# Performance work log

Measured on AMD Instinct MI355X. Metric: run time of the kernel, lower is better.

## Reference

```python
import jax, jax.numpy as jnp
import numpy as np

B = 8192
IN = 2048
H = 2048


def setup_inputs() -> dict:
    key = jax.random.key(0)
    ks = jax.random.split(key, 16)
    s_in = 1.0 / np.sqrt(IN)
    s_h = 1.0 / np.sqrt(H)
    inp = {
        "x": jax.random.normal(ks[0], (B, IN), jnp.float32),
        "h": jax.random.normal(ks[1], (B, H), jnp.float32),
        "c": jax.random.normal(ks[2], (B, H), jnp.float32),
        # Linear weights stored torch-style as [out, in]
        "w_xf": jax.random.uniform(ks[3], (H, IN), jnp.float32, -s_in, s_in),
        "w_hf": jax.random.uniform(ks[4], (H, H), jnp.float32, -s_h, s_h),
        "b_f": jax.random.normal(ks[5], (H,), jnp.float32),
        "w_xi": jax.random.uniform(ks[6], (H, IN), jnp.float32, -s_in, s_in),
        "w_hi": jax.random.uniform(ks[7], (H, H), jnp.float32, -s_h, s_h),
        "b_i": jax.random.normal(ks[8], (H,), jnp.float32),
        "w_xo": jax.random.uniform(ks[9], (H, IN), jnp.float32, -s_in, s_in),
        "w_ho": jax.random.uniform(ks[10], (H, H), jnp.float32, -s_h, s_h),
        "b_o": jax.random.normal(ks[11], (H,), jnp.float32),
        "w_xc": jax.random.uniform(ks[12], (H, IN), jnp.float32, -s_in, s_in),
        "w_hc": jax.random.uniform(ks[13], (H, H), jnp.float32, -s_h, s_h),
        "b_c": jax.random.normal(ks[14], (H,), jnp.float32),
    }
    return inp


def reference(x, h, c, w_xf, w_hf, b_f, w_xi, w_hi, b_i,
              w_xo, w_ho, b_o, w_xc, w_hc, b_c):
    # Fuse the 8 small GEMMs into 2 batched GEMMs (x-side, h-side).
    Wx = jnp.concatenate([w_xf, w_xi, w_xo, w_xc], axis=0)  # [4H, IN]
    Wh = jnp.concatenate([w_hf, w_hi, w_ho, w_hc], axis=0)  # [4H, H]
    b = jnp.concatenate([b_f, b_i, b_o, b_c], axis=0)       # [4H]
    gates = x @ Wx.T + h @ Wh.T + b                          # [B, 4H]
    hd = h.shape[-1]
    f = jax.nn.sigmoid(gates[:, 0 * hd:1 * hd])
    i = jax.nn.sigmoid(gates[:, 1 * hd:2 * hd])
    o = jax.nn.sigmoid(gates[:, 2 * hd:3 * hd])
    c_tilde = jnp.tanh(gates[:, 3 * hd:4 * hd])
    c_new = f * c + i * c_tilde
    h_new = o * jnp.tanh(c_new)
    return (h_new, c_new)
```

## Files before the change

kernel.cpp:

```cpp
#include <hip/hip_runtime.h>


typedef __attribute__((ext_vector_type(8))) short short8;
typedef __attribute__((ext_vector_type(8))) __bf16 bf16x8;
typedef __attribute__((ext_vector_type(4))) float f32x4;

#define GLDS(gp, lp)                                                        \
  __builtin_amdgcn_global_load_lds(                                         \
      (const __attribute__((address_space(1))) void*)(gp),                  \
      (__attribute__((address_space(3))) void*)(lp), 16, 0, 0)

__device__ __forceinline__ unsigned short f2bf(float f) {
  unsigned u = __builtin_bit_cast(unsigned, f);
  u = (u + 0x7FFFu + ((u >> 16) & 1u)) >> 16;
  return (unsigned short)u;
}

__global__ void pack_x_kernel(const float* __restrict__ x,
                              const float* __restrict__ h,
                              short* __restrict__ X2) {
  long tid = (long)blockIdx.x * blockDim.x + threadIdx.x;
  long flat = tid * 8;
  int row = (int)(flat >> 12);
  int k = (int)(flat & 4095);
  const float* src = (k < 2048) ? (x + (long)row * 2048 + k)
                                : (h + (long)row * 2048 + (k - 2048));
  float4 a = *(const float4*)src;
  float4 b = *(const float4*)(src + 4);
  short8 o;
  o[0] = (short)f2bf(a.x); o[1] = (short)f2bf(a.y);
  o[2] = (short)f2bf(a.z); o[3] = (short)f2bf(a.w);
  o[4] = (short)f2bf(b.x); o[5] = (short)f2bf(b.y);
  o[6] = (short)f2bf(b.z); o[7] = (short)f2bf(b.w);
  *(short8*)(X2 + flat) = o;
}

__global__ void pack_w_kernel(const float* __restrict__ wxf, const float* __restrict__ wxi,
                              const float* __restrict__ wxo, const float* __restrict__ wxc,
                              const float* __restrict__ whf, const float* __restrict__ whi,
                              const float* __restrict__ who, const float* __restrict__ whc,
                              short* __restrict__ W3) {
  long tid = (long)blockIdx.x * blockDim.x + threadIdx.x;
  long flat = tid * 8;
  int j = (int)(flat >> 12);
  int k = (int)(flat & 4095);
  int hc = ((j >> 6) << 4) | (j & 15);
  int g = (j >> 4) & 3;
  const float* base;
  if (k < 2048) {
    const float* wx = (g == 0) ? wxf : (g == 1) ? wxi : (g == 2) ? wxo : wxc;
    base = wx + (long)hc * 2048 + k;
  } else {
    const float* wh = (g == 0) ? whf : (g == 1) ? whi : (g == 2) ? who : whc;
    base = wh + (long)hc * 2048 + (k - 2048);
  }
  float4 a = *(const float4*)base;
  float4 b = *(const float4*)(base + 4);
  short8 o;
  o[0] = (short)f2bf(a.x); o[1] = (short)f2bf(a.y);
  o[2] = (short)f2bf(a.z); o[3] = (short)f2bf(a.w);
  o[4] = (short)f2bf(b.x); o[5] = (short)f2bf(b.y);
  o[6] = (short)f2bf(b.z); o[7] = (short)f2bf(b.w);
  *(short8*)(W3 + flat) = o;
}

__global__ __launch_bounds__(512, 2) void lstm_fused_gemm(
    const short* __restrict__ X2, const short* __restrict__ W3,
    const float* __restrict__ cin,
    const float* __restrict__ bF, const float* __restrict__ bI,
    const float* __restrict__ bO, const float* __restrict__ bC,
    float* __restrict__ hout, float* __restrict__ cout_) {
  __shared__ __align__(16) short lds[65536];

  const int tid = threadIdx.x;
  const int lane = tid & 63;
  const int w = tid >> 6;
  const int wm = w >> 2;
  const int wn = w & 3;

  const int bid = blockIdx.x;
  const int bM = (bid & 7) * 4 + ((bid >> 3) & 3);
  const int bN = bid >> 5;

  const int ci = w * 64 + lane;
  const int r0 = ci >> 2;
  const int ss = (ci & 3) ^ ((r0 >> 1) & 3);
  const short* aRow0 = X2 + ((size_t)(bM * 256 + r0)) * 4096 + ss * 8;
  const short* aRow1 = aRow0 + (size_t)128 * 4096;
  const short* bRow0 = W3 + ((size_t)(bN * 256 + r0)) * 4096 + ss * 8;
  const short* bRow1 = bRow0 + (size_t)128 * 4096;
  const int wOff = w * 1024;

#define STAGE2(q, tt, bb) do {                                               \
    const int _kh = (q) >> 1;                                                \
    const short* _g0; const short* _g1;                                      \
    if ((q) == 0 || (q) == 2) {                                              \
      _g0 = aRow0 + (tt) * 64 + _kh * 32;                                    \
      _g1 = aRow1 + (tt) * 64 + _kh * 32;                                    \
    } else {                                                                 \
      _g0 = bRow0 + (tt) * 64 + _kh * 32;                                    \
      _g1 = bRow1 + (tt) * 64 + _kh * 32;                                    \
    }                                                                        \
    char* _l0 = (char*)lds + (bb) * 65536 + (q) * 16384 + wOff;              \
    GLDS(_g0, _l0);                                                          \
    GLDS(_g1, _l0 + 8192);                                                   \
  } while (0)

  const int lr = lane & 15, hi = lane >> 4;
  const int swz = ((hi ^ ((lr >> 1) & 3)) << 4);
  const int aoff = wm * 8192 + lr * 64 + swz;
  const int boff = 16384 + wn * 4096 + lr * 64 + swz;

#define LDSRD(off) (*(const bf16x8*)((const char*)lds + (off)))
#define MFMA_(a, b, c) __builtin_amdgcn_mfma_f32_16x16x32_bf16((a), (b), (c), 0, 0, 0)

  f32x4 acc[8][4] = {};

  STAGE2(0, 0, 0); STAGE2(1, 0, 0); STAGE2(3, 0, 0); STAGE2(2, 0, 0);
  asm volatile("s_waitcnt vmcnt(0)" ::: "memory");
  __builtin_amdgcn_s_barrier();

#pragma unroll 2
  for (int t = 0; t < 64; ++t) {
    const int cur = t & 1, nxt = cur ^ 1;
    const int bo = cur << 16;
    const int t1 = (t + 1) & 63;
    bf16x8 a[4], b[4];

#pragma unroll
    for (int i = 0; i < 4; ++i) a[i] = LDSRD(bo + aoff + i * 1024);
#pragma unroll
    for (int n = 0; n < 4; ++n) b[n] = LDSRD(bo + boff + n * 1024);
    STAGE2(0, t1, nxt);
    STAGE2(1, t1, nxt);
    STAGE2(3, t1, nxt);
    __builtin_amdgcn_s_barrier();
    __builtin_amdgcn_s_setprio(1);
#pragma unroll
    for (int n = 0; n < 4; ++n)
#pragma unroll
      for (int i = 0; i < 4; ++i) acc[i][n] = MFMA_(a[i], b[n], acc[i][n]);
    __builtin_amdgcn_s_setprio(0);

#pragma unroll
    for (int i = 0; i < 4; ++i) a[i] = LDSRD(bo + aoff + (4 + i) * 1024);
    STAGE2(2, t1, nxt);
    asm volatile("s_waitcnt vmcnt(8)" ::: "memory");
    __builtin_amdgcn_s_barrier();
    __builtin_amdgcn_s_setprio(1);
#pragma unroll
    for (int n = 0; n < 4; ++n)
#pragma unroll
      for (int i = 0; i < 4; ++i) acc[4 + i][n] = MFMA_(a[i], b[n], acc[4 + i][n]);
    __builtin_amdgcn_s_setprio(0);

#pragma unroll
    for (int i = 0; i < 4; ++i) a[i] = LDSRD(bo + aoff + 32768 + i * 1024);
#pragma unroll
    for (int n = 0; n < 4; ++n) b[n] = LDSRD(bo + boff + 32768 + n * 1024);
    __builtin_amdgcn_s_barrier();
    __builtin_amdgcn_s_setprio(1);
#pragma unroll
    for (int n = 0; n < 4; ++n)
#pragma unroll
      for (int i = 0; i < 4; ++i) acc[i][n] = MFMA_(a[i], b[n], acc[i][n]);
    __builtin_amdgcn_s_setprio(0);

#pragma unroll
    for (int i = 0; i < 4; ++i) a[i] = LDSRD(bo + aoff + 32768 + (4 + i) * 1024);
    asm volatile("s_waitcnt vmcnt(4)" ::: "memory");
    __builtin_amdgcn_s_barrier();
    __builtin_amdgcn_s_setprio(1);
#pragma unroll
    for (int n = 0; n < 4; ++n)
#pragma unroll
      for (int i = 0; i < 4; ++i) acc[4 + i][n] = MFMA_(a[i], b[n], acc[4 + i][n]);
    __builtin_amdgcn_s_setprio(0);
  }

  const int hc = bN * 64 + wn * 16 + lr;
  const float vbf = bF[hc], vbi = bI[hc], vbo = bO[hc], vbc = bC[hc];
#pragma unroll
  for (int m = 0; m < 8; ++m) {
    const int rbase = bM * 256 + wm * 128 + m * 16 + hi * 4;
#pragma unroll
    for (int v = 0; v < 4; ++v) {
      const size_t idx = (size_t)(rbase + v) * 2048 + hc;
      float gf = acc[m][0][v] + vbf;
      float gi = acc[m][1][v] + vbi;
      float go = acc[m][2][v] + vbo;
      float gc = acc[m][3][v] + vbc;
      float fg = 1.f / (1.f + __expf(-gf));
      float ig = 1.f / (1.f + __expf(-gi));
      float og = 1.f / (1.f + __expf(-go));
      float ct = 2.f / (1.f + __expf(-2.f * gc)) - 1.f;
      float cn = fg * cin[idx] + ig * ct;
      float hn = og * (2.f / (1.f + __expf(-2.f * cn)) - 1.f);
      hout[idx] = hn;
      cout_[idx] = cn;
    }
  }
}

extern "C" void kernel_launch(void* const* d_in, const int* in_sizes, int n_in,
                              void* d_out, int out_size, void* d_ws, size_t ws_size,
                              hipStream_t stream) {
  const float* x    = (const float*)d_in[0];
  const float* h    = (const float*)d_in[1];
  const float* c    = (const float*)d_in[2];
  const float* w_xf = (const float*)d_in[3];
  const float* w_hf = (const float*)d_in[4];
  const float* b_f  = (const float*)d_in[5];
  const float* w_xi = (const float*)d_in[6];
  const float* w_hi = (const float*)d_in[7];
  const float* b_i  = (const float*)d_in[8];
  const float* w_xo = (const float*)d_in[9];
  const float* w_ho = (const float*)d_in[10];
  const float* b_o  = (const float*)d_in[11];
  const float* w_xc = (const float*)d_in[12];
  const float* w_hc = (const float*)d_in[13];
  const float* b_c  = (const float*)d_in[14];

  float* hout  = (float*)d_out;
  float* cout_ = hout + (size_t)8192 * 2048;

  short* X2 = (short*)d_ws;
  short* W3 = X2 + (size_t)8192 * 4096;

  const int packBlocks = (int)(((long)8192 * 4096 / 8) / 256);
  pack_x_kernel<<<packBlocks, 256, 0, stream>>>(x, h, X2);
  pack_w_kernel<<<packBlocks, 256, 0, stream>>>(w_xf, w_xi, w_xo, w_xc,
                                                w_hf, w_hi, w_ho, w_hc, W3);

  lstm_fused_gemm<<<1024, 512, 0, stream>>>(X2, W3, c, b_f, b_i, b_o, b_c,
                                            hout, cout_);
}
```

Before: 543.0 us.

## Make GEMM persistent over four N tiles with cross-tile prefetch and rebalanced staging

The launch shrinks from 1024 to 256 blocks, and each block now loops over four N tiles (stride 8) with the same M tile, running the LSTM epilogue and resetting accumulators between tiles. The last K step of each tile prefetches the next tile's first slice, so the pipeline does not drain between tiles. The four quarter-stages are now issued one per MFMA phase instead of three up front, with adjusted vmcnt waits. The goal is to cut launch and tail overhead and smooth memory issue. The risk is that 256 blocks may underfill the GPU's CUs at two blocks per CU, and the epilogue is serialized inside the loop.

```diff
diff --git a/kernel.cpp b/kernel.cpp
--- a/kernel.cpp
+++ b/kernel.cpp
@@ -80,26 +80,27 @@
 
   const int bid = blockIdx.x;
   const int bM = (bid & 7) * 4 + ((bid >> 3) & 3);
-  const int bN = bid >> 5;
+  const int bN0 = (bid >> 3) >> 2;
 
   const int ci = w * 64 + lane;
   const int r0 = ci >> 2;
   const int ss = (ci & 3) ^ ((r0 >> 1) & 3);
   const short* aRow0 = X2 + ((size_t)(bM * 256 + r0)) * 4096 + ss * 8;
   const short* aRow1 = aRow0 + (size_t)128 * 4096;
-  const short* bRow0 = W3 + ((size_t)(bN * 256 + r0)) * 4096 + ss * 8;
-  const short* bRow1 = bRow0 + (size_t)128 * 4096;
+  const size_t bStride = (size_t)8 * 256 * 4096;
+  const short* bBase0 = W3 + ((size_t)(bN0 * 256 + r0)) * 4096 + ss * 8;
+  const short* bBase1 = bBase0 + (size_t)128 * 4096;
   const int wOff = w * 1024;
 
-#define STAGE2(q, tt, bb) do {                                               \
+#define STAGEQ(q, tt, bb, B0, B1) do {                                       \
     const int _kh = (q) >> 1;                                                \
     const short* _g0; const short* _g1;                                      \
     if ((q) == 0 || (q) == 2) {                                              \
       _g0 = aRow0 + (tt) * 64 + _kh * 32;                                    \
       _g1 = aRow1 + (tt) * 64 + _kh * 32;                                    \
     } else {                                                                 \
-      _g0 = bRow0 + (tt) * 64 + _kh * 32;                                    \
-      _g1 = bRow1 + (tt) * 64 + _kh * 32;                                    \
+      _g0 = (B0) + (tt) * 64 + _kh * 32;                                     \
+      _g1 = (B1) + (tt) * 64 + _kh * 32;                                     \
     }                                                                        \
     char* _l0 = (char*)lds + (bb) * 65536 + (q) * 16384 + wOff;              \
     GLDS(_g0, _l0);                                                          \
@@ -116,89 +117,107 @@
 
   f32x4 acc[8][4] = {};
 
-  STAGE2(0, 0, 0); STAGE2(1, 0, 0); STAGE2(3, 0, 0); STAGE2(2, 0, 0);
+  STAGEQ(0, 0, 0, bBase0, bBase1);
+  STAGEQ(1, 0, 0, bBase0, bBase1);
+  STAGEQ(2, 0, 0, bBase0, bBase1);
+  STAGEQ(3, 0, 0, bBase0, bBase1);
   asm volatile("s_waitcnt vmcnt(0)" ::: "memory");
   __builtin_amdgcn_s_barrier();
 
+  for (int j = 0; j < 4; ++j) {
+    const short* bR0 = bBase0 + (size_t)j * bStride;
+    const short* bR1 = bBase1 + (size_t)j * bStride;
+    const short* bR0n = (j < 3) ? (bR0 + bStride) : bR0;
+    const short* bR1n = (j < 3) ? (bR1 + bStride) : bR1;
+
 #pragma unroll 2
-  for (int t = 0; t < 64; ++t) {
-    const int cur = t & 1, nxt = cur ^ 1;
-    const int bo = cur << 16;
-    const int t1 = (t + 1) & 63;
-    bf16x8 a[4], b[4];
-
-#pragma unroll
-    for (int i = 0; i < 4; ++i) a[i] = LDSRD(bo + aoff + i * 1024);
-#pragma unroll
-    for (int n = 0; n < 4; ++n) b[n] = LDSRD(bo + boff + n * 1024);
-    STAGE2(0, t1, nxt);
-    STAGE2(1, t1, nxt);
-    STAGE2(3, t1, nxt);
-    __builtin_amdgcn_s_barrier();
-    __builtin_amdgcn_s_setprio(1);
-#pragma unroll
-    for (int n = 0; n < 4; ++n)
-#pragma unroll
-      for (int i = 0; i < 4; ++i) acc[i][n] = MFMA_(a[i], b[n], acc[i][n]);
-    __builtin_amdgcn_s_setprio(0);
-
-#pragma unroll
-    for (int i = 0; i < 4; ++i) a[i] = LDSRD(bo + aoff + (4 + i) * 1024);
-    STAGE2(2, t1, nxt);
-    asm volatile("s_waitcnt vmcnt(8)" ::: "memory");
-    __builtin_amdgcn_s_barrier();
-    __builtin_amdgcn_s_setprio(1);
-#pragma unroll
-    for (int n = 0; n < 4; ++n)
-#pragma unroll
-      for (int i = 0; i < 4; ++i) acc[4 + i][n] = MFMA_(a[i], b[n], acc[4 + i][n]);
-    __builtin_amdgcn_s_setprio(0);
-
-#pragma unroll
-    for (int i = 0; i < 4; ++i) a[i] = LDSRD(bo + aoff + 32768 + i * 1024);
-#pragma unroll
-    for (int n = 0; n < 4; ++n) b[n] = LDSRD(bo + boff + 32768 + n * 1024);
-    __builtin_amdgcn_s_barrier();
-    __builtin_amdgcn_s_setprio(1);
-#pragma unroll
-    for (int n = 0; n < 4; ++n)
-#pragma unroll
-      for (int i = 0; i < 4; ++i) acc[i][n] = MFMA_(a[i], b[n], acc[i][n]);
-    __builtin_amdgcn_s_setprio(0);
-
-#pragma unroll
-    for (int i = 0; i < 4; ++i) a[i] = LDSRD(bo + aoff + 32768 + (4 + i) * 1024);
-    asm volatile("s_waitcnt vmcnt(4)" ::: "memory");
-    __builtin_amdgcn_s_barrier();
-    __builtin_amdgcn_s_setprio(1);
-#pragma unroll
-    for (int n = 0; n < 4; ++n)
-#pragma unroll
-      for (int i = 0; i < 4; ++i) acc[4 + i][n] = MFMA_(a[i], b[n], acc[4 + i][n]);
-    __builtin_amdgcn_s_setprio(0);
-  }
-
-  const int hc = bN * 64 + wn * 16 + lr;
-  const float vbf = bF[hc], vbi = bI[hc], vbo = bO[hc], vbc = bC[hc];
-#pragma unroll
-  for (int m = 0; m < 8; ++m) {
-    const int rbase = bM * 256 + wm * 128 + m * 16 + hi * 4;
-#pragma unroll
-    for (int v = 0; v < 4; ++v) {
-      const size_t idx = (size_t)(rbase + v) * 2048 + hc;
-      float gf = acc[m][0][v] + vbf;
-      float gi = acc[m][1][v] + vbi;
-      float go = acc[m][2][v] + vbo;
-      float gc = acc[m][3][v] + vbc;
-      float fg = 1.f / (1.f + __expf(-gf));
-      float ig = 1.f / (1.f + __expf(-gi));
-      float og = 1.f / (1.f + __expf(-go));
-      float ct = 2.f / (1.f + __expf(-2.f * gc)) - 1.f;
-      float cn = fg * cin[idx] + ig * ct;
-      float hn = og * (2.f / (1.f + __expf(-2.f * cn)) - 1.f);
-      hout[idx] = hn;
-      cout_[idx] = cn;
+    for (int t = 0; t < 64; ++t) {
+      const int cur = t & 1, nxt = cur ^ 1;
+      const int bo = cur << 16;
+      const bool last = (t == 63);
+      const int tt = last ? 0 : t + 1;
+      const short* sB0 = last ? bR0n : bR0;
+      const short* sB1 = last ? bR1n : bR1;
+      bf16x8 a[4], b[4];
+
+#pragma unroll
+      for (int i = 0; i < 4; ++i) a[i] = LDSRD(bo + aoff + i * 1024);
+#pragma unroll
+      for (int n = 0; n < 4; ++n) b[n] = LDSRD(bo + boff + n * 1024);
+      STAGEQ(0, tt, nxt, sB0, sB1);
+      __builtin_amdgcn_s_barrier();
+      __builtin_amdgcn_s_setprio(1);
+#pragma unroll
+      for (int n = 0; n < 4; ++n)
+#pragma unroll
+        for (int i = 0; i < 4; ++i) acc[i][n] = MFMA_(a[i], b[n], acc[i][n]);
+      __builtin_amdgcn_s_setprio(0);
+
+#pragma unroll
+      for (int i = 0; i < 4; ++i) a[i] = LDSRD(bo + aoff + (4 + i) * 1024);
+      STAGEQ(1, tt, nxt, sB0, sB1);
+      asm volatile("s_waitcnt vmcnt(6)" ::: "memory");
+      __builtin_amdgcn_s_barrier();
+      __builtin_amdgcn_s_setprio(1);
+#pragma unroll
+      for (int n = 0; n < 4; ++n)
+#pragma unroll
+        for (int i = 0; i < 4; ++i) acc[4 + i][n] = MFMA_(a[i], b[n], acc[4 + i][n]);
+      __builtin_amdgcn_s_setprio(0);
+
+#pragma unroll
+      for (int i = 0; i < 4; ++i) a[i] = LDSRD(bo + aoff + 32768 + i * 1024);
+#pragma unroll
+      for (int n = 0; n < 4; ++n) b[n] = LDSRD(bo + boff + 32768 + n * 1024);
+      STAGEQ(2, tt, nxt, sB0, sB1);
+      asm volatile("s_waitcnt vmcnt(6)" ::: "memory");
+      __builtin_amdgcn_s_barrier();
+      __builtin_amdgcn_s_setprio(1);
+#pragma unroll
+      for (int n = 0; n < 4; ++n)
+#pragma unroll
+        for (int i = 0; i < 4; ++i) acc[i][n] = MFMA_(a[i], b[n], acc[i][n]);
+      __builtin_amdgcn_s_setprio(0);
+
+#pragma unroll
+      for (int i = 0; i < 4; ++i) a[i] = LDSRD(bo + aoff + 32768 + (4 + i) * 1024);
+      STAGEQ(3, tt, nxt, sB0, sB1);
+      asm volatile("s_waitcnt vmcnt(4)" ::: "memory");
+      __builtin_amdgcn_s_barrier();
+      __builtin_amdgcn_s_setprio(1);
+#pragma unroll
+      for (int n = 0; n < 4; ++n)
+#pragma unroll
+        for (int i = 0; i < 4; ++i) acc[4 + i][n] = MFMA_(a[i], b[n], acc[4 + i][n]);
+      __builtin_amdgcn_s_setprio(0);
     }
+
+    const int hc = (bN0 + j * 8) * 64 + wn * 16 + lr;
+    const float vbf = bF[hc], vbi = bI[hc], vbo = bO[hc], vbc = bC[hc];
+#pragma unroll
+    for (int m = 0; m < 8; ++m) {
+      const int rbase = bM * 256 + wm * 128 + m * 16 + hi * 4;
+#pragma unroll
+      for (int v = 0; v < 4; ++v) {
+        const size_t idx = (size_t)(rbase + v) * 2048 + hc;
+        float gf = acc[m][0][v] + vbf;
+        float gi = acc[m][1][v] + vbi;
+        float go = acc[m][2][v] + vbo;
+        float gc = acc[m][3][v] + vbc;
+        float fg = 1.f / (1.f + __expf(-gf));
+        float ig = 1.f / (1.f + __expf(-gi));
+        float og = 1.f / (1.f + __expf(-go));
+        float ct = 2.f / (1.f + __expf(-2.f * gc)) - 1.f;
+        float cn = fg * cin[idx] + ig * ct;
+        float hn = og * (2.f / (1.f + __expf(-2.f * cn)) - 1.f);
+        hout[idx] = hn;
+        cout_[idx] = cn;
+      }
+    }
+#pragma unroll
+    for (int m = 0; m < 8; ++m)
+#pragma unroll
+      for (int n = 0; n < 4; ++n) acc[m][n] = (f32x4)(0.f);
   }
 }
 
@@ -232,6 +251,6 @@
   pack_w_kernel<<<packBlocks, 256, 0, stream>>>(w_xf, w_xi, w_xo, w_xc,
                                                 w_hf, w_hi, w_ho, w_hc, W3);
 
-  lstm_fused_gemm<<<1024, 512, 0, stream>>>(X2, W3, c, b_f, b_i, b_o, b_c,
-                                            hout, cout_);
-}
+  lstm_fused_gemm<<<256, 512, 0, stream>>>(X2, W3, c, b_f, b_i, b_o, b_c,
+                                           hout, cout_);
+}
```

Result: slower. 571.8 us (+5.3%).

## Switch fused LSTM GEMM to 32x32x16 MFMA with new LDS swizzle

Applied to the files above, without the earlier changes.

Replaces the 16x16x32 bf16 MFMA tiles with 32x32x16 MFMAs, so each wave holds a 4x2 grid of 32x32 accumulators. The LDS staging layout and swizzle are rewritten around row pairs, and the K loop is split into four stages with one global-to-LDS quarter load per stage. The epilogue uses lane shuffles to gather the four gate values so that half the lanes write h and half write c. The larger MFMA shape cuts LDS reads per flop and instruction count. In exchange it changes register pressure, bank-conflict behaviour and the pipeline wait points.

```diff
diff --git a/kernel.cpp b/kernel.cpp
--- a/kernel.cpp
+++ b/kernel.cpp
@@ -3,7 +3,7 @@
 
 typedef __attribute__((ext_vector_type(8))) short short8;
 typedef __attribute__((ext_vector_type(8))) __bf16 bf16x8;
-typedef __attribute__((ext_vector_type(4))) float f32x4;
+typedef __attribute__((ext_vector_type(16))) float f32x16;
 
 #define GLDS(gp, lp)                                                        \
   __builtin_amdgcn_global_load_lds(                                         \
@@ -82,41 +82,46 @@
   const int bM = (bid & 7) * 4 + ((bid >> 3) & 3);
   const int bN = bid >> 5;
 
-  const int ci = w * 64 + lane;
-  const int r0 = ci >> 2;
-  const int ss = (ci & 3) ^ ((r0 >> 1) & 3);
-  const short* aRow0 = X2 + ((size_t)(bM * 256 + r0)) * 4096 + ss * 8;
+  const int sPair = tid >> 3;
+  const int sSlog = (tid & 7) ^ (sPair & 7);
+  const int srow = sPair * 2 + (sSlog >> 2);
+  const int skoff = (sSlog & 3) * 8;
+  const short* aRow0 = X2 + ((size_t)(bM * 256 + srow)) * 4096 + skoff;
   const short* aRow1 = aRow0 + (size_t)128 * 4096;
-  const short* bRow0 = W3 + ((size_t)(bN * 256 + r0)) * 4096 + ss * 8;
+  const short* bRow0 = W3 + ((size_t)(bN * 256 + srow)) * 4096 + skoff;
   const short* bRow1 = bRow0 + (size_t)128 * 4096;
-  const int wOff = w * 1024;
-
-#define STAGE2(q, tt, bb) do {                                               \
+
+#define STAGEQ(q, tt, bb) do {                                               \
     const int _kh = (q) >> 1;                                                \
     const short* _g0; const short* _g1;                                      \
-    if ((q) == 0 || (q) == 2) {                                              \
+    if (((q) & 1) == 0) {                                                    \
       _g0 = aRow0 + (tt) * 64 + _kh * 32;                                    \
       _g1 = aRow1 + (tt) * 64 + _kh * 32;                                    \
     } else {                                                                 \
       _g0 = bRow0 + (tt) * 64 + _kh * 32;                                    \
       _g1 = bRow1 + (tt) * 64 + _kh * 32;                                    \
     }                                                                        \
-    char* _l0 = (char*)lds + (bb) * 65536 + (q) * 16384 + wOff;              \
+    char* _l0 = (char*)lds + (bb) * 65536 + (q) * 16384 + tid * 16;          \
     GLDS(_g0, _l0);                                                          \
     GLDS(_g1, _l0 + 8192);                                                   \
   } while (0)
 
-  const int lr = lane & 15, hi = lane >> 4;
-  const int swz = ((hi ^ ((lr >> 1) & 3)) << 4);
-  const int aoff = wm * 8192 + lr * 64 + swz;
-  const int boff = 16384 + wn * 4096 + lr * 64 + swz;
+  const int l31 = lane & 31, hi2 = lane >> 5;
+  const int rA = wm * 128 + l31;
+  const int pA = rA >> 1;
+  const int aoffE = pA * 128 + ((((rA & 1) * 4) + 0 + hi2) ^ (pA & 7)) * 16;
+  const int aoffO = pA * 128 + ((((rA & 1) * 4) + 2 + hi2) ^ (pA & 7)) * 16;
+  const int rB = wn * 64 + l31;
+  const int pB = rB >> 1;
+  const int boffE = 16384 + pB * 128 + ((((rB & 1) * 4) + 0 + hi2) ^ (pB & 7)) * 16;
+  const int boffO = 16384 + pB * 128 + ((((rB & 1) * 4) + 2 + hi2) ^ (pB & 7)) * 16;
 
 #define LDSRD(off) (*(const bf16x8*)((const char*)lds + (off)))
-#define MFMA_(a, b, c) __builtin_amdgcn_mfma_f32_16x16x32_bf16((a), (b), (c), 0, 0, 0)
-
-  f32x4 acc[8][4] = {};
-
-  STAGE2(0, 0, 0); STAGE2(1, 0, 0); STAGE2(3, 0, 0); STAGE2(2, 0, 0);
+#define MFMA32(a, b, c) __builtin_amdgcn_mfma_f32_32x32x16_bf16((a), (b), (c), 0, 0, 0)
+
+  f32x16 acc[4][2] = {};
+
+  STAGEQ(0, 0, 0); STAGEQ(1, 0, 0); STAGEQ(2, 0, 0); STAGEQ(3, 0, 0);
   asm volatile("s_waitcnt vmcnt(0)" ::: "memory");
   __builtin_amdgcn_s_barrier();
 
@@ -125,79 +130,91 @@
     const int cur = t & 1, nxt = cur ^ 1;
     const int bo = cur << 16;
     const int t1 = (t + 1) & 63;
-    bf16x8 a[4], b[4];
-
-#pragma unroll
-    for (int i = 0; i < 4; ++i) a[i] = LDSRD(bo + aoff + i * 1024);
-#pragma unroll
-    for (int n = 0; n < 4; ++n) b[n] = LDSRD(bo + boff + n * 1024);
-    STAGE2(0, t1, nxt);
-    STAGE2(1, t1, nxt);
-    STAGE2(3, t1, nxt);
-    __builtin_amdgcn_s_barrier();
-    __builtin_amdgcn_s_setprio(1);
-#pragma unroll
-    for (int n = 0; n < 4; ++n)
-#pragma unroll
-      for (int i = 0; i < 4; ++i) acc[i][n] = MFMA_(a[i], b[n], acc[i][n]);
-    __builtin_amdgcn_s_setprio(0);
-
-#pragma unroll
-    for (int i = 0; i < 4; ++i) a[i] = LDSRD(bo + aoff + (4 + i) * 1024);
-    STAGE2(2, t1, nxt);
-    asm volatile("s_waitcnt vmcnt(8)" ::: "memory");
-    __builtin_amdgcn_s_barrier();
-    __builtin_amdgcn_s_setprio(1);
-#pragma unroll
-    for (int n = 0; n < 4; ++n)
-#pragma unroll
-      for (int i = 0; i < 4; ++i) acc[4 + i][n] = MFMA_(a[i], b[n], acc[4 + i][n]);
-    __builtin_amdgcn_s_setprio(0);
-
-#pragma unroll
-    for (int i = 0; i < 4; ++i) a[i] = LDSRD(bo + aoff + 32768 + i * 1024);
-#pragma unroll
-    for (int n = 0; n < 4; ++n) b[n] = LDSRD(bo + boff + 32768 + n * 1024);
-    __builtin_amdgcn_s_barrier();
-    __builtin_amdgcn_s_setprio(1);
-#pragma unroll
-    for (int n = 0; n < 4; ++n)
-#pragma unroll
-      for (int i = 0; i < 4; ++i) acc[i][n] = MFMA_(a[i], b[n], acc[i][n]);
-    __builtin_amdgcn_s_setprio(0);
-
-#pragma unroll
-    for (int i = 0; i < 4; ++i) a[i] = LDSRD(bo + aoff + 32768 + (4 + i) * 1024);
+    bf16x8 a[4], b[2];
+
+#pragma unroll
+    for (int m = 0; m < 4; ++m) a[m] = LDSRD(bo + aoffE + m * 2048);
+#pragma unroll
+    for (int n = 0; n < 2; ++n) b[n] = LDSRD(bo + boffE + n * 2048);
+    STAGEQ(0, t1, nxt);
+    __builtin_amdgcn_s_barrier();
+    __builtin_amdgcn_s_setprio(1);
+#pragma unroll
+    for (int n = 0; n < 2; ++n)
+#pragma unroll
+      for (int m = 0; m < 4; ++m) acc[m][n] = MFMA32(a[m], b[n], acc[m][n]);
+    __builtin_amdgcn_s_setprio(0);
+
+#pragma unroll
+    for (int m = 0; m < 4; ++m) a[m] = LDSRD(bo + aoffO + m * 2048);
+#pragma unroll
+    for (int n = 0; n < 2; ++n) b[n] = LDSRD(bo + boffO + n * 2048);
+    STAGEQ(1, t1, nxt);
     asm volatile("s_waitcnt vmcnt(4)" ::: "memory");
     __builtin_amdgcn_s_barrier();
     __builtin_amdgcn_s_setprio(1);
 #pragma unroll
-    for (int n = 0; n < 4; ++n)
-#pragma unroll
-      for (int i = 0; i < 4; ++i) acc[4 + i][n] = MFMA_(a[i], b[n], acc[4 + i][n]);
+    for (int n = 0; n < 2; ++n)
+#pragma unroll
+      for (int m = 0; m < 4; ++m) acc[m][n] = MFMA32(a[m], b[n], acc[m][n]);
+    __builtin_amdgcn_s_setprio(0);
+
+#pragma unroll
+    for (int m = 0; m < 4; ++m) a[m] = LDSRD(bo + 32768 + aoffE + m * 2048);
+#pragma unroll
+    for (int n = 0; n < 2; ++n) b[n] = LDSRD(bo + 32768 + boffE + n * 2048);
+    STAGEQ(2, t1, nxt);
+    __builtin_amdgcn_s_barrier();
+    __builtin_amdgcn_s_setprio(1);
+#pragma unroll
+    for (int n = 0; n < 2; ++n)
+#pragma unroll
+      for (int m = 0; m < 4; ++m) acc[m][n] = MFMA32(a[m], b[n], acc[m][n]);
+    __builtin_amdgcn_s_setprio(0);
+
+#pragma unroll
+    for (int m = 0; m < 4; ++m) a[m] = LDSRD(bo + 32768 + aoffO + m * 2048);
+#pragma unroll
+    for (int n = 0; n < 2; ++n) b[n] = LDSRD(bo + 32768 + boffO + n * 2048);
+    STAGEQ(3, t1, nxt);
+    asm volatile("s_waitcnt vmcnt(4)" ::: "memory");
+    __builtin_amdgcn_s_barrier();
+    __builtin_amdgcn_s_setprio(1);
+#pragma unroll
+    for (int n = 0; n < 2; ++n)
+#pragma unroll
+      for (int m = 0; m < 4; ++m) acc[m][n] = MFMA32(a[m], b[n], acc[m][n]);
     __builtin_amdgcn_s_setprio(0);
   }
 
-  const int hc = bN * 64 + wn * 16 + lr;
-  const float vbf = bF[hc], vbi = bI[hc], vbo = bO[hc], vbc = bC[hc];
-#pragma unroll
-  for (int m = 0; m < 8; ++m) {
-    const int rbase = bM * 256 + wm * 128 + m * 16 + hi * 4;
-#pragma unroll
-    for (int v = 0; v < 4; ++v) {
-      const size_t idx = (size_t)(rbase + v) * 2048 + hc;
-      float gf = acc[m][0][v] + vbf;
-      float gi = acc[m][1][v] + vbi;
-      float go = acc[m][2][v] + vbo;
-      float gc = acc[m][3][v] + vbc;
-      float fg = 1.f / (1.f + __expf(-gf));
-      float ig = 1.f / (1.f + __expf(-gi));
-      float og = 1.f / (1.f + __expf(-go));
-      float ct = 2.f / (1.f + __expf(-2.f * gc)) - 1.f;
-      float cn = fg * cin[idx] + ig * ct;
-      float hn = og * (2.f / (1.f + __expf(-2.f * cn)) - 1.f);
-      hout[idx] = hn;
-      cout_[idx] = cn;
+  const int l15 = lane & 15;
+  const int bit4 = (lane >> 4) & 1;
+  const int hc = (bN * 4 + wn) * 16 + l15;
+  const float vbF = bF[hc], vbI = bI[hc], vbO = bO[hc], vbC = bC[hc];
+  float* const cPtr = cout_;
+#pragma unroll
+  for (int m = 0; m < 4; ++m) {
+    const int rowbase = bM * 256 + wm * 128 + m * 32 + 4 * hi2;
+#pragma unroll
+    for (int r = 0; r < 16; ++r) {
+      const int rowg = rowbase + (r & 3) + 8 * (r >> 2);
+      const float a0 = acc[m][0][r];
+      const float a1 = acc[m][1][r];
+      const float s0 = __shfl_xor(a0, 16);
+      const float s1 = __shfl_xor(a1, 16);
+      const float gf = (bit4 ? s0 : a0) + vbF;
+      const float gi = (bit4 ? a0 : s0) + vbI;
+      const float go = (bit4 ? s1 : a1) + vbO;
+      const float gc = (bit4 ? a1 : s1) + vbC;
+      const float fg = 1.f / (1.f + __expf(-gf));
+      const float ig = 1.f / (1.f + __expf(-gi));
+      const float og = 1.f / (1.f + __expf(-go));
+      const float ct = 2.f / (1.f + __expf(-2.f * gc)) - 1.f;
+      const size_t idx = (size_t)rowg * 2048 + hc;
+      const float cn = fg * cin[idx] + ig * ct;
+      const float hn = og * (2.f / (1.f + __expf(-2.f * cn)) - 1.f);
+      float* dst = bit4 ? cPtr : hout;
+      dst[idx] = bit4 ? cn : hn;
     }
   }
 }
```

New measurement: 637.3 us. 1.17x slower.

## Load A operand directly from global into registers, stage only B in LDS

Applied to the files above, without the earlier changes.

The A tile (activations) is no longer staged through LDS. Each wave now loads its own A fragments straight from global memory into registers, double-buffered across k-halves. Only the B (weight) tile still goes through global_load_lds, so LDS use is halved and the LDS read traffic for A disappears. The cost is more global load instructions and register pressure, and A rows are reused only within a wave rather than across the four wn waves sharing them, which raises L2/global traffic. The vmcnt waits are recalibrated for the new mix of loads.

```diff
diff --git a/kernel.cpp b/kernel.cpp
--- a/kernel.cpp
+++ b/kernel.cpp
@@ -70,7 +70,7 @@
     const float* __restrict__ bF, const float* __restrict__ bI,
     const float* __restrict__ bO, const float* __restrict__ bC,
     float* __restrict__ hout, float* __restrict__ cout_) {
-  __shared__ __align__(16) short lds[65536];
+  __shared__ __align__(16) short lds[32768];
 
   const int tid = threadIdx.x;
   const int lane = tid & 63;
@@ -82,99 +82,93 @@
   const int bM = (bid & 7) * 4 + ((bid >> 3) & 3);
   const int bN = bid >> 5;
 
-  const int ci = w * 64 + lane;
-  const int r0 = ci >> 2;
-  const int ss = (ci & 3) ^ ((r0 >> 1) & 3);
-  const short* aRow0 = X2 + ((size_t)(bM * 256 + r0)) * 4096 + ss * 8;
-  const short* aRow1 = aRow0 + (size_t)128 * 4096;
+  const int r0 = tid >> 2;
+  const int ss = (tid & 3) ^ ((r0 >> 1) & 3);
   const short* bRow0 = W3 + ((size_t)(bN * 256 + r0)) * 4096 + ss * 8;
   const short* bRow1 = bRow0 + (size_t)128 * 4096;
-  const int wOff = w * 1024;
-
-#define STAGE2(q, tt, bb) do {                                               \
-    const int _kh = (q) >> 1;                                                \
-    const short* _g0; const short* _g1;                                      \
-    if ((q) == 0 || (q) == 2) {                                              \
-      _g0 = aRow0 + (tt) * 64 + _kh * 32;                                    \
-      _g1 = aRow1 + (tt) * 64 + _kh * 32;                                    \
-    } else {                                                                 \
-      _g0 = bRow0 + (tt) * 64 + _kh * 32;                                    \
-      _g1 = bRow1 + (tt) * 64 + _kh * 32;                                    \
-    }                                                                        \
-    char* _l0 = (char*)lds + (bb) * 65536 + (q) * 16384 + wOff;              \
-    GLDS(_g0, _l0);                                                          \
-    GLDS(_g1, _l0 + 8192);                                                   \
+
+#define STAGE_B(kk, tt, bb) do {                                             \
+    GLDS(bRow0 + (tt) * 64 + (kk) * 32,                                      \
+         (char*)lds + (bb) + (kk) * 16384 + tid * 16);                       \
+    GLDS(bRow1 + (tt) * 64 + (kk) * 32,                                      \
+         (char*)lds + (bb) + (kk) * 16384 + 8192 + tid * 16);                \
   } while (0)
 
   const int lr = lane & 15, hi = lane >> 4;
-  const int swz = ((hi ^ ((lr >> 1) & 3)) << 4);
-  const int aoff = wm * 8192 + lr * 64 + swz;
-  const int boff = 16384 + wn * 4096 + lr * 64 + swz;
+  const int R0 = wn * 64 + lr;
+  const int fB = (R0 >> 1) & 3;
+  const int bbase = R0 * 64 + ((hi ^ fB) << 4);
+
+  const short* aBase = X2 + ((size_t)(bM * 256 + wm * 128 + lr)) * 4096 + hi * 8;
+#define ALOAD(dst, mh, kk, tt)                                               \
+  do {                                                                       \
+    _Pragma("unroll")                                                        \
+    for (int mi = 0; mi < 4; ++mi)                                           \
+      dst[mi] = *(const bf16x8*)(aBase + (size_t)((mh) * 64 + mi * 16) * 4096 \
+                                 + (tt) * 64 + (kk) * 32);                   \
+  } while (0)
 
 #define LDSRD(off) (*(const bf16x8*)((const char*)lds + (off)))
 #define MFMA_(a, b, c) __builtin_amdgcn_mfma_f32_16x16x32_bf16((a), (b), (c), 0, 0, 0)
 
   f32x4 acc[8][4] = {};
-
-  STAGE2(0, 0, 0); STAGE2(1, 0, 0); STAGE2(3, 0, 0); STAGE2(2, 0, 0);
-  asm volatile("s_waitcnt vmcnt(0)" ::: "memory");
+  bf16x8 aP[4], aQ[4];
+  bf16x8 b0[4], b1[4];
+
+  STAGE_B(0, 0, 0);
+  STAGE_B(1, 0, 0);
+  ALOAD(aP, 0, 0, 0);
+  asm volatile("s_waitcnt vmcnt(4)" ::: "memory");
   __builtin_amdgcn_s_barrier();
 
 #pragma unroll 2
   for (int t = 0; t < 64; ++t) {
-    const int cur = t & 1, nxt = cur ^ 1;
-    const int bo = cur << 16;
+    const int bo = (t & 1) * 32768;
+    const int bon = bo ^ 32768;
     const int t1 = (t + 1) & 63;
-    bf16x8 a[4], b[4];
-
-#pragma unroll
-    for (int i = 0; i < 4; ++i) a[i] = LDSRD(bo + aoff + i * 1024);
-#pragma unroll
-    for (int n = 0; n < 4; ++n) b[n] = LDSRD(bo + boff + n * 1024);
-    STAGE2(0, t1, nxt);
-    STAGE2(1, t1, nxt);
-    STAGE2(3, t1, nxt);
-    __builtin_amdgcn_s_barrier();
-    __builtin_amdgcn_s_setprio(1);
-#pragma unroll
-    for (int n = 0; n < 4; ++n)
-#pragma unroll
-      for (int i = 0; i < 4; ++i) acc[i][n] = MFMA_(a[i], b[n], acc[i][n]);
-    __builtin_amdgcn_s_setprio(0);
-
-#pragma unroll
-    for (int i = 0; i < 4; ++i) a[i] = LDSRD(bo + aoff + (4 + i) * 1024);
-    STAGE2(2, t1, nxt);
-    asm volatile("s_waitcnt vmcnt(8)" ::: "memory");
-    __builtin_amdgcn_s_barrier();
-    __builtin_amdgcn_s_setprio(1);
-#pragma unroll
-    for (int n = 0; n < 4; ++n)
-#pragma unroll
-      for (int i = 0; i < 4; ++i) acc[4 + i][n] = MFMA_(a[i], b[n], acc[4 + i][n]);
-    __builtin_amdgcn_s_setprio(0);
-
-#pragma unroll
-    for (int i = 0; i < 4; ++i) a[i] = LDSRD(bo + aoff + 32768 + i * 1024);
-#pragma unroll
-    for (int n = 0; n < 4; ++n) b[n] = LDSRD(bo + boff + 32768 + n * 1024);
-    __builtin_amdgcn_s_barrier();
-    __builtin_amdgcn_s_setprio(1);
-#pragma unroll
-    for (int n = 0; n < 4; ++n)
-#pragma unroll
-      for (int i = 0; i < 4; ++i) acc[i][n] = MFMA_(a[i], b[n], acc[i][n]);
-    __builtin_amdgcn_s_setprio(0);
-
-#pragma unroll
-    for (int i = 0; i < 4; ++i) a[i] = LDSRD(bo + aoff + 32768 + (4 + i) * 1024);
-    asm volatile("s_waitcnt vmcnt(4)" ::: "memory");
-    __builtin_amdgcn_s_barrier();
-    __builtin_amdgcn_s_setprio(1);
-#pragma unroll
-    for (int n = 0; n < 4; ++n)
-#pragma unroll
-      for (int i = 0; i < 4; ++i) acc[4 + i][n] = MFMA_(a[i], b[n], acc[4 + i][n]);
+
+#pragma unroll
+    for (int n = 0; n < 4; ++n) b0[n] = LDSRD(bo + bbase + n * 1024);
+    ALOAD(aQ, 1, 0, t);
+    STAGE_B(0, t1, bon);
+    __builtin_amdgcn_s_barrier();
+    __builtin_amdgcn_s_setprio(1);
+#pragma unroll
+    for (int n = 0; n < 4; ++n)
+#pragma unroll
+      for (int mi = 0; mi < 4; ++mi) acc[mi][n] = MFMA_(aP[mi], b0[n], acc[mi][n]);
+    __builtin_amdgcn_s_setprio(0);
+
+#pragma unroll
+    for (int n = 0; n < 4; ++n) b1[n] = LDSRD(bo + 16384 + bbase + n * 1024);
+    ALOAD(aP, 0, 1, t);
+    STAGE_B(1, t1, bon);
+    asm volatile("s_waitcnt vmcnt(20)" ::: "memory");
+    __builtin_amdgcn_s_barrier();
+    __builtin_amdgcn_s_setprio(1);
+#pragma unroll
+    for (int n = 0; n < 4; ++n)
+#pragma unroll
+      for (int mi = 0; mi < 4; ++mi) acc[4 + mi][n] = MFMA_(aQ[mi], b0[n], acc[4 + mi][n]);
+    __builtin_amdgcn_s_setprio(0);
+
+    ALOAD(aQ, 1, 1, t);
+    __builtin_amdgcn_s_barrier();
+    __builtin_amdgcn_s_setprio(1);
+#pragma unroll
+    for (int n = 0; n < 4; ++n)
+#pragma unroll
+      for (int mi = 0; mi < 4; ++mi) acc[mi][n] = MFMA_(aP[mi], b1[n], acc[mi][n]);
+    __builtin_amdgcn_s_setprio(0);
+
+    ALOAD(aP, 0, 0, t1);
+    asm volatile("s_waitcnt vmcnt(14)" ::: "memory");
+    __builtin_amdgcn_s_barrier();
+    __builtin_amdgcn_s_setprio(1);
+#pragma unroll
+    for (int n = 0; n < 4; ++n)
+#pragma unroll
+      for (int mi = 0; mi < 4; ++mi) acc[4 + mi][n] = MFMA_(aQ[mi], b1[n], acc[4 + mi][n]);
     __builtin_amdgcn_s_setprio(0);
   }
 
```

After: 1.089 ms. 2.01x slower.
